# Kernel tuning notes

Measured on AMD Instinct MI355X. Metric: run time of the kernel, lower is better.

Reference implementation:

```python
import jax, jax.numpy as jnp
import numpy as np

M, N, E = 4096, 100, 128


def setup_inputs() -> dict:
    key = jax.random.key(0)
    ks = jax.random.split(key, 14)
    s = 0.05
    return {
        "user": jax.random.normal(ks[0], (M, E), jnp.float32),
        "item": jax.random.normal(ks[1], (M, E), jnp.float32),
        "pus": jax.random.normal(ks[2], (M, N, E), jnp.float32),
        "pis": jax.random.normal(ks[3], (M, N, E), jnp.float32),
        "pss": jax.random.normal(ks[4], (M, N, E), jnp.float32),
        "C": jax.random.normal(ks[5], (M, N, E), jnp.float32),
        # l1: Linear(3E -> E) + ReLU
        "W1": jax.random.normal(ks[6], (3 * E, E), jnp.float32) * s,
        "b1": jnp.zeros((E,), jnp.float32),
        # l2: Linear(E -> 1), no activation
        "W2": jax.random.normal(ks[7], (E, 1), jnp.float32) * s,
        "b2": jnp.zeros((1,), jnp.float32),
        # lR: Linear(2E -> E) + ReLU
        "WR": jax.random.normal(ks[8], (2 * E, E), jnp.float32) * s,
        "bR": jnp.zeros((E,), jnp.float32),
        # lout: Linear(E -> E) + ReLU
        "Wo": jax.random.normal(ks[9], (E, E), jnp.float32) * s,
        "bo": jnp.zeros((E,), jnp.float32),
    }


def reference(user, item, pus, pis, pss, C, W1, b1, W2, b2, WR, bR, Wo, bo):
    # additive attention scores over paths
    h = jax.nn.relu(jnp.concatenate((pus, pis, pss), axis=-1) @ W1 + b1)  # [M,N,E]
    scores = h @ W2 + b2                                                  # [M,N,1]
    w = jax.nn.softmax(scores, axis=-2)                                   # softmax over N paths
    w = jnp.swapaxes(w, -1, -2)                                           # [M,1,N]
    # value transform and weighted pooling over paths
    v = jax.nn.relu(jnp.concatenate((C, pss), axis=-1) @ WR + bR)         # [M,N,E]
    pair_emb = jnp.matmul(w, v)                                           # [M,1,E]
    pair_emb = jax.nn.relu(pair_emb @ Wo + bo)                            # lout
    return pair_emb.reshape((C.shape[-3], Wo.shape[-1]))                  # [M,E]
```

## Files before the change

kernel.cpp:

```cpp
#include <hip/hip_runtime.h>
#include <hip/hip_bf16.h>


#define M_ 4096
#define N_ 100
#define E_ 128

typedef __bf16 bf16x8 __attribute__((ext_vector_type(8)));
typedef float  f32x4  __attribute__((ext_vector_type(4)));

#define GLOAD_LDS16(g, l)                                                    \
  __builtin_amdgcn_global_load_lds(                                          \
      (const __attribute__((address_space(1))) void*)(g),                    \
      (__attribute__((address_space(3))) void*)(l), 16, 0, 0)

__global__ void prep_weights(const float* __restrict__ W1, const float* __restrict__ WR,
                             __bf16* __restrict__ W1t, __bf16* __restrict__ WRt) {
    int i = blockIdx.x * 256 + threadIdx.x;
    if (i < 384 * 128) {
        int n = i / 384, k = i % 384;
        W1t[i] = (__bf16)W1[k * 128 + n];
    } else {
        int j = i - 384 * 128;
        if (j < 256 * 128) {
            int n = j / 256, k = j % 256;
            WRt[j] = (__bf16)WR[k * 128 + n];
        }
    }
}

__global__ __launch_bounds__(256, 2) void fused(
    const float* __restrict__ pus, const float* __restrict__ pis,
    const float* __restrict__ pss, const float* __restrict__ Cc,
    const __bf16* __restrict__ W1t, const float* __restrict__ b1,
    const float* __restrict__ W2, const float* __restrict__ b2,
    const __bf16* __restrict__ WRt, const float* __restrict__ bR,
    const float* __restrict__ Wo, const float* __restrict__ bo,
    float* __restrict__ out)
{
    __shared__ __align__(16) __bf16 Xs[2][128][64];
    __shared__ __align__(16) __bf16 Ws[2][128][64];
    __shared__ float part[2][128];
    __shared__ float sLDS[128];
    __shared__ float wLDS[128];
    __shared__ float pairLDS[128];

    const int tid  = threadIdx.x;
    const int lane = tid & 63;
    const int wid  = tid >> 6;
    const int wr = wid >> 1, wc = wid & 1;
    const int m = blockIdx.x;
    const long base = (long)m * (N_ * E_);

    float w2v[4], b1v[4], bRv[4];
    #pragma unroll
    for (int b = 0; b < 4; ++b) {
        int col = wc * 64 + b * 16 + (lane & 15);
        w2v[b] = W2[col]; b1v[b] = b1[col]; bRv[b] = bR[col];
    }
    const float b2v = b2[0];

    float4 xvE[8], xvO[8];

    auto fetchX = [&](float4 (&xv)[8], int step) {
        const float* __restrict__ src =
            (step < 2) ? pus : (step < 4) ? pis : (step < 6) ? pss
          : (step < 8) ? Cc : pss;
        const int colbase = (step & 1) << 6;
        #pragma unroll
        for (int i = 0; i < 8; ++i) {
            int c  = tid + 256 * i;
            int r  = c >> 4;
            int rc = (r < N_) ? r : (N_ - 1);
            int k4 = (c & 15) << 2;
            xv[i] = *reinterpret_cast<const float4*>(
                src + base + (long)rc * E_ + colbase + k4);
        }
    };
    auto writeX = [&](float4 (&xv)[8], int buf) {
        #pragma unroll
        for (int i = 0; i < 8; ++i) {
            int c  = tid + 256 * i;
            int r  = c >> 4;
            int k4 = (c & 15) << 2;
            int blk  = k4 >> 3;
            int phys = ((blk ^ (r & 7)) << 3) + (k4 & 7);
            union { __bf16 h[4]; uint2 u; } tw;
            tw.h[0] = (__bf16)xv[i].x; tw.h[1] = (__bf16)xv[i].y;
            tw.h[2] = (__bf16)xv[i].z; tw.h[3] = (__bf16)xv[i].w;
            *reinterpret_cast<uint2*>(&Xs[buf][r][phys]) = tw.u;
        }
    };
    auto stageW = [&](int step, int buf) {
        const __bf16* __restrict__ Wt = (step < 6) ? W1t : WRt;
        const int wstride = (step < 6) ? 384 : 256;
        const int k0 = (step < 6) ? step * 64 : (step - 6) * 64;
        #pragma unroll
        for (int j = 0; j < 4; ++j) {
            int chunk = wid * 4 + j;
            int n  = chunk * 8 + (lane >> 3);
            int kb = (lane & 7) ^ (n & 7);
            GLOAD_LDS16(Wt + n * wstride + k0 + (kb << 3), &Ws[buf][chunk * 8][0]);
        }
    };

    f32x4 acc[4][4] = {};

    fetchX(xvE, 0);
    fetchX(xvO, 1);
    stageW(0, 0);
    __builtin_amdgcn_sched_barrier(0);
    writeX(xvE, 0);
    fetchX(xvE, 2);
    __builtin_amdgcn_sched_barrier(0);
    asm volatile("s_waitcnt lgkmcnt(0)" ::: "memory");
    asm volatile("s_waitcnt vmcnt(8)" ::: "memory");
    __builtin_amdgcn_s_barrier();

    #pragma unroll
    for (int s = 0; s < 10; ++s) {
        const int cur = s & 1;

        if (s < 9) {
            stageW(s + 1, cur ^ 1);
            __builtin_amdgcn_sched_barrier(0);
            if (((s + 1) & 1) == 0) {
                writeX(xvE, cur ^ 1);
                if (s + 3 < 10) fetchX(xvE, s + 3);
            } else {
                writeX(xvO, cur ^ 1);
                if (s + 3 < 10) fetchX(xvO, s + 3);
            }
            __builtin_amdgcn_sched_barrier(0);
        }

        #pragma unroll
        for (int ks = 0; ks < 2; ++ks) {
            const int g = lane >> 4;
            const int kblk = (ks << 2) + g;
            bf16x8 af[4], bfr[4];
            #pragma unroll
            for (int a = 0; a < 4; ++a) {
                int rr = wr * 64 + a * 16 + (lane & 15);
                af[a] = *reinterpret_cast<const bf16x8*>(&Xs[cur][rr][(kblk ^ (rr & 7)) << 3]);
            }
            #pragma unroll
            for (int b = 0; b < 4; ++b) {
                int nn = wc * 64 + b * 16 + (lane & 15);
                bfr[b] = *reinterpret_cast<const bf16x8*>(&Ws[cur][nn][(kblk ^ (nn & 7)) << 3]);
            }
            #pragma unroll
            for (int a = 0; a < 4; ++a)
                #pragma unroll
                for (int b = 0; b < 4; ++b)
                    acc[a][b] = __builtin_amdgcn_mfma_f32_16x16x32_bf16(
                        af[a], bfr[b], acc[a][b], 0, 0, 0);
        }

        if (s == 5) {
            #pragma unroll
            for (int a = 0; a < 4; ++a) {
                #pragma unroll
                for (int r = 0; r < 4; ++r) {
                    float ps = 0.f;
                    #pragma unroll
                    for (int b = 0; b < 4; ++b) {
                        float h = fmaxf(acc[a][b][r] + b1v[b], 0.f);
                        ps += h * w2v[b];
                    }
                    ps += __shfl_xor(ps, 1);
                    ps += __shfl_xor(ps, 2);
                    ps += __shfl_xor(ps, 4);
                    ps += __shfl_xor(ps, 8);
                    if ((lane & 15) == 0) {
                        int row = wr * 64 + a * 16 + ((lane >> 4) << 2) + r;
                        part[wc][row] = ps;
                    }
                }
            }
            asm volatile("s_waitcnt lgkmcnt(0)" ::: "memory");
            __builtin_amdgcn_s_barrier();
            if (tid < 128) sLDS[tid] = part[0][tid] + part[1][tid] + b2v;
            asm volatile("s_waitcnt lgkmcnt(0)" ::: "memory");
            __builtin_amdgcn_s_barrier();
            if (wid == 0) {
                float s0 = (lane < N_) ? sLDS[lane] : -3e38f;
                float s1 = (lane + 64 < N_) ? sLDS[lane + 64] : -3e38f;
                float mx = fmaxf(s0, s1);
                #pragma unroll
                for (int off = 1; off < 64; off <<= 1) mx = fmaxf(mx, __shfl_xor(mx, off));
                float e0 = (lane < N_) ? __expf(s0 - mx) : 0.f;
                float e1 = (lane + 64 < N_) ? __expf(s1 - mx) : 0.f;
                float sum = e0 + e1;
                #pragma unroll
                for (int off = 1; off < 64; off <<= 1) sum += __shfl_xor(sum, off);
                float inv = 1.f / sum;
                wLDS[lane]      = e0 * inv;
                wLDS[lane + 64] = e1 * inv;
            }
            #pragma unroll
            for (int a = 0; a < 4; ++a)
                #pragma unroll
                for (int b = 0; b < 4; ++b)
                    #pragma unroll
                    for (int q = 0; q < 4; ++q)
                        acc[a][b][q] = 0.f;
        }

        asm volatile("s_waitcnt lgkmcnt(0)" ::: "memory");
        if (s < 7) asm volatile("s_waitcnt vmcnt(8)" ::: "memory");
        else       asm volatile("s_waitcnt vmcnt(0)" ::: "memory");
        __builtin_amdgcn_s_barrier();
    }

    {
        float psum[4] = {0.f, 0.f, 0.f, 0.f};
        const int g = lane >> 4;
        #pragma unroll
        for (int a = 0; a < 4; ++a) {
            #pragma unroll
            for (int r = 0; r < 4; ++r) {
                int row = wr * 64 + a * 16 + g * 4 + r;
                float wgt = wLDS[row];
                #pragma unroll
                for (int b = 0; b < 4; ++b) {
                    float v = fmaxf(acc[a][b][r] + bRv[b], 0.f);
                    psum[b] += wgt * v;
                }
            }
        }
        #pragma unroll
        for (int b = 0; b < 4; ++b) {
            psum[b] += __shfl_xor(psum[b], 16);
            psum[b] += __shfl_xor(psum[b], 32);
        }
        if (lane < 16) {
            #pragma unroll
            for (int b = 0; b < 4; ++b)
                part[wr][wc * 64 + b * 16 + lane] = psum[b];
        }
        __syncthreads();
        if (tid < 128) pairLDS[tid] = part[0][tid] + part[1][tid];
        __syncthreads();
        if (tid < 128) {
            float o = bo[tid];
            #pragma unroll 8
            for (int k = 0; k < 128; ++k)
                o += pairLDS[k] * Wo[k * 128 + tid];
            out[(long)m * 128 + tid] = fmaxf(o, 0.f);
        }
    }
}

extern "C" void kernel_launch(void* const* d_in, const int* in_sizes, int n_in,
                              void* d_out, int out_size, void* d_ws, size_t ws_size,
                              hipStream_t stream) {
    const float* pus = (const float*)d_in[2];
    const float* pis = (const float*)d_in[3];
    const float* pss = (const float*)d_in[4];
    const float* C   = (const float*)d_in[5];
    const float* W1  = (const float*)d_in[6];
    const float* b1  = (const float*)d_in[7];
    const float* W2  = (const float*)d_in[8];
    const float* b2  = (const float*)d_in[9];
    const float* WR  = (const float*)d_in[10];
    const float* bR  = (const float*)d_in[11];
    const float* Wo  = (const float*)d_in[12];
    const float* bo  = (const float*)d_in[13];
    (void)in_sizes; (void)n_in; (void)ws_size;

    __bf16* W1t = (__bf16*)d_ws;
    __bf16* WRt = W1t + 384 * 128;

    prep_weights<<<320, 256, 0, stream>>>(W1, WR, W1t, WRt);
    fused<<<M_, 256, 0, stream>>>(pus, pis, pss, C, W1t, b1, W2, b2,
                                  WRt, bR, Wo, bo, (float*)d_out);
}
```

Before: 222.0 us.

## Use 8-wave blocks and load weight fragments directly from global memory

Doubles the block size to 512 threads with a 2x4 wave grid, halving per-thread accumulators and X fetch registers. Weight tiles are no longer staged into LDS via global_load_lds; each wave loads its bf16 weight fragments straight from global memory (L2) into registers. This aims to raise parallelism and cut LDS footprint, at the cost of repeated L2 weight reads and coarser synchronisation on the X prefetch.

```diff
diff --git a/kernel.cpp b/kernel.cpp
--- a/kernel.cpp
+++ b/kernel.cpp
@@ -8,11 +8,6 @@
 
 typedef __bf16 bf16x8 __attribute__((ext_vector_type(8)));
 typedef float  f32x4  __attribute__((ext_vector_type(4)));
-
-#define GLOAD_LDS16(g, l)                                                    \
-  __builtin_amdgcn_global_load_lds(                                          \
-      (const __attribute__((address_space(1))) void*)(g),                    \
-      (__attribute__((address_space(3))) void*)(l), 16, 0, 0)
 
 __global__ void prep_weights(const float* __restrict__ W1, const float* __restrict__ WR,
                              __bf16* __restrict__ W1t, __bf16* __restrict__ WRt) {
@@ -29,7 +24,7 @@
     }
 }
 
-__global__ __launch_bounds__(256, 2) void fused(
+__global__ __launch_bounds__(512, 4) void fused(
     const float* __restrict__ pus, const float* __restrict__ pis,
     const float* __restrict__ pss, const float* __restrict__ Cc,
     const __bf16* __restrict__ W1t, const float* __restrict__ b1,
@@ -39,8 +34,7 @@
     float* __restrict__ out)
 {
     __shared__ __align__(16) __bf16 Xs[2][128][64];
-    __shared__ __align__(16) __bf16 Ws[2][128][64];
-    __shared__ float part[2][128];
+    __shared__ float part[4][128];
     __shared__ float sLDS[128];
     __shared__ float wLDS[128];
     __shared__ float pairLDS[128];
@@ -48,28 +42,29 @@
     const int tid  = threadIdx.x;
     const int lane = tid & 63;
     const int wid  = tid >> 6;
-    const int wr = wid >> 1, wc = wid & 1;
+    const int wr = wid >> 2, wc = wid & 3;
+    const int g  = lane >> 4;
     const int m = blockIdx.x;
     const long base = (long)m * (N_ * E_);
 
-    float w2v[4], b1v[4], bRv[4];
+    float w2v[2], b1v[2], bRv[2];
     #pragma unroll
-    for (int b = 0; b < 4; ++b) {
-        int col = wc * 64 + b * 16 + (lane & 15);
+    for (int b = 0; b < 2; ++b) {
+        int col = wc * 32 + b * 16 + (lane & 15);
         w2v[b] = W2[col]; b1v[b] = b1[col]; bRv[b] = bR[col];
     }
     const float b2v = b2[0];
 
-    float4 xvE[8], xvO[8];
-
-    auto fetchX = [&](float4 (&xv)[8], int step) {
+    float4 xvE[4], xvO[4];
+
+    auto fetchX = [&](float4 (&xv)[4], int step) {
         const float* __restrict__ src =
             (step < 2) ? pus : (step < 4) ? pis : (step < 6) ? pss
           : (step < 8) ? Cc : pss;
         const int colbase = (step & 1) << 6;
         #pragma unroll
-        for (int i = 0; i < 8; ++i) {
-            int c  = tid + 256 * i;
+        for (int i = 0; i < 4; ++i) {
+            int c  = tid + 512 * i;
             int r  = c >> 4;
             int rc = (r < N_) ? r : (N_ - 1);
             int k4 = (c & 15) << 2;
@@ -77,10 +72,10 @@
                 src + base + (long)rc * E_ + colbase + k4);
         }
     };
-    auto writeX = [&](float4 (&xv)[8], int buf) {
-        #pragma unroll
-        for (int i = 0; i < 8; ++i) {
-            int c  = tid + 256 * i;
+    auto writeX = [&](float4 (&xv)[4], int buf) {
+        #pragma unroll
+        for (int i = 0; i < 4; ++i) {
+            int c  = tid + 512 * i;
             int r  = c >> 4;
             int k4 = (c & 15) << 2;
             int blk  = k4 >> 3;
@@ -91,39 +86,37 @@
             *reinterpret_cast<uint2*>(&Xs[buf][r][phys]) = tw.u;
         }
     };
-    auto stageW = [&](int step, int buf) {
-        const __bf16* __restrict__ Wt = (step < 6) ? W1t : WRt;
-        const int wstride = (step < 6) ? 384 : 256;
-        const int k0 = (step < 6) ? step * 64 : (step - 6) * 64;
-        #pragma unroll
-        for (int j = 0; j < 4; ++j) {
-            int chunk = wid * 4 + j;
-            int n  = chunk * 8 + (lane >> 3);
-            int kb = (lane & 7) ^ (n & 7);
-            GLOAD_LDS16(Wt + n * wstride + k0 + (kb << 3), &Ws[buf][chunk * 8][0]);
-        }
-    };
-
-    f32x4 acc[4][4] = {};
+
+    f32x4 acc[4][2] = {};
 
     fetchX(xvE, 0);
     fetchX(xvO, 1);
-    stageW(0, 0);
-    __builtin_amdgcn_sched_barrier(0);
     writeX(xvE, 0);
     fetchX(xvE, 2);
+    asm volatile("s_waitcnt lgkmcnt(0)" ::: "memory");
+    __builtin_amdgcn_s_barrier();
     __builtin_amdgcn_sched_barrier(0);
-    asm volatile("s_waitcnt lgkmcnt(0)" ::: "memory");
-    asm volatile("s_waitcnt vmcnt(8)" ::: "memory");
-    __builtin_amdgcn_s_barrier();
 
     #pragma unroll
     for (int s = 0; s < 10; ++s) {
         const int cur = s & 1;
 
+        const __bf16* __restrict__ Wt = (s < 6) ? W1t : WRt;
+        const int wstride = (s < 6) ? 384 : 256;
+        const int k0 = (s < 6) ? s * 64 : (s - 6) * 64;
+        bf16x8 wf[2][2];
+        #pragma unroll
+        for (int ks = 0; ks < 2; ++ks) {
+            const int kblk = (ks << 2) + g;
+            #pragma unroll
+            for (int b = 0; b < 2; ++b) {
+                int nn = wc * 32 + b * 16 + (lane & 15);
+                wf[ks][b] = *reinterpret_cast<const bf16x8*>(
+                    Wt + nn * wstride + k0 + (kblk << 3));
+            }
+        }
+
         if (s < 9) {
-            stageW(s + 1, cur ^ 1);
-            __builtin_amdgcn_sched_barrier(0);
             if (((s + 1) & 1) == 0) {
                 writeX(xvE, cur ^ 1);
                 if (s + 3 < 10) fetchX(xvE, s + 3);
@@ -131,30 +124,24 @@
                 writeX(xvO, cur ^ 1);
                 if (s + 3 < 10) fetchX(xvO, s + 3);
             }
-            __builtin_amdgcn_sched_barrier(0);
         }
 
         #pragma unroll
         for (int ks = 0; ks < 2; ++ks) {
-            const int g = lane >> 4;
             const int kblk = (ks << 2) + g;
-            bf16x8 af[4], bfr[4];
+            bf16x8 af[4];
             #pragma unroll
             for (int a = 0; a < 4; ++a) {
                 int rr = wr * 64 + a * 16 + (lane & 15);
-                af[a] = *reinterpret_cast<const bf16x8*>(&Xs[cur][rr][(kblk ^ (rr & 7)) << 3]);
-            }
-            #pragma unroll
-            for (int b = 0; b < 4; ++b) {
-                int nn = wc * 64 + b * 16 + (lane & 15);
-                bfr[b] = *reinterpret_cast<const bf16x8*>(&Ws[cur][nn][(kblk ^ (nn & 7)) << 3]);
+                af[a] = *reinterpret_cast<const bf16x8*>(
+                    &Xs[cur][rr][(kblk ^ (rr & 7)) << 3]);
             }
             #pragma unroll
             for (int a = 0; a < 4; ++a)
                 #pragma unroll
-                for (int b = 0; b < 4; ++b)
+                for (int b = 0; b < 2; ++b)
                     acc[a][b] = __builtin_amdgcn_mfma_f32_16x16x32_bf16(
-                        af[a], bfr[b], acc[a][b], 0, 0, 0);
+                        af[a], wf[ks][b], acc[a][b], 0, 0, 0);
         }
 
         if (s == 5) {
@@ -164,7 +151,7 @@
                 for (int r = 0; r < 4; ++r) {
                     float ps = 0.f;
                     #pragma unroll
-                    for (int b = 0; b < 4; ++b) {
+                    for (int b = 0; b < 2; ++b) {
                         float h = fmaxf(acc[a][b][r] + b1v[b], 0.f);
                         ps += h * w2v[b];
                     }
@@ -173,16 +160,20 @@
                     ps += __shfl_xor(ps, 4);
                     ps += __shfl_xor(ps, 8);
                     if ((lane & 15) == 0) {
-                        int row = wr * 64 + a * 16 + ((lane >> 4) << 2) + r;
+                        int row = wr * 64 + a * 16 + g * 4 + r;
                         part[wc][row] = ps;
                     }
                 }
             }
             asm volatile("s_waitcnt lgkmcnt(0)" ::: "memory");
             __builtin_amdgcn_s_barrier();
-            if (tid < 128) sLDS[tid] = part[0][tid] + part[1][tid] + b2v;
+            __builtin_amdgcn_sched_barrier(0);
+            if (tid < 128)
+                sLDS[tid] = part[0][tid] + part[1][tid] + part[2][tid]
+                          + part[3][tid] + b2v;
             asm volatile("s_waitcnt lgkmcnt(0)" ::: "memory");
             __builtin_amdgcn_s_barrier();
+            __builtin_amdgcn_sched_barrier(0);
             if (wid == 0) {
                 float s0 = (lane < N_) ? sLDS[lane] : -3e38f;
                 float s1 = (lane + 64 < N_) ? sLDS[lane + 64] : -3e38f;
@@ -201,21 +192,19 @@
             #pragma unroll
             for (int a = 0; a < 4; ++a)
                 #pragma unroll
-                for (int b = 0; b < 4; ++b)
+                for (int b = 0; b < 2; ++b)
                     #pragma unroll
                     for (int q = 0; q < 4; ++q)
                         acc[a][b][q] = 0.f;
         }
 
         asm volatile("s_waitcnt lgkmcnt(0)" ::: "memory");
-        if (s < 7) asm volatile("s_waitcnt vmcnt(8)" ::: "memory");
-        else       asm volatile("s_waitcnt vmcnt(0)" ::: "memory");
         __builtin_amdgcn_s_barrier();
+        __builtin_amdgcn_sched_barrier(0);
     }
 
     {
-        float psum[4] = {0.f, 0.f, 0.f, 0.f};
-        const int g = lane >> 4;
+        float psum[2] = {0.f, 0.f};
         #pragma unroll
         for (int a = 0; a < 4; ++a) {
             #pragma unroll
@@ -223,21 +212,21 @@
                 int row = wr * 64 + a * 16 + g * 4 + r;
                 float wgt = wLDS[row];
                 #pragma unroll
-                for (int b = 0; b < 4; ++b) {
+                for (int b = 0; b < 2; ++b) {
                     float v = fmaxf(acc[a][b][r] + bRv[b], 0.f);
                     psum[b] += wgt * v;
                 }
             }
         }
         #pragma unroll
-        for (int b = 0; b < 4; ++b) {
+        for (int b = 0; b < 2; ++b) {
             psum[b] += __shfl_xor(psum[b], 16);
             psum[b] += __shfl_xor(psum[b], 32);
         }
         if (lane < 16) {
             #pragma unroll
-            for (int b = 0; b < 4; ++b)
-                part[wr][wc * 64 + b * 16 + lane] = psum[b];
+            for (int b = 0; b < 2; ++b)
+                part[wr][wc * 32 + b * 16 + lane] = psum[b];
         }
         __syncthreads();
         if (tid < 128) pairLDS[tid] = part[0][tid] + part[1][tid];
@@ -273,6 +262,6 @@
     __bf16* WRt = W1t + 384 * 128;
 
     prep_weights<<<320, 256, 0, stream>>>(W1, WR, W1t, WRt);
-    fused<<<M_, 256, 0, stream>>>(pus, pis, pss, C, W1t, b1, W2, b2,
+    fused<<<M_, 512, 0, stream>>>(pus, pis, pss, C, W1t, b1, W2, b2,
                                   WRt, bR, Wo, bo, (float*)d_out);
 }
```

Result: slower. 283.7 us (+27.8%).
